# Optimization experiments

Hardware: AMD Instinct MI355X
Metric: run time of the kernel (lower is better)

## Reference

```python
import jax, jax.numpy as jnp
import numpy as np

P, K, T, C, F = 2048, 8, 32, 16384, 128  # paths, channels/path, steps/channel, channels, feature


def setup_inputs() -> dict:
    key = jax.random.key(0)
    k0, k1, k2, k3, k4, k5, k6 = jax.random.split(key, 7)
    s = 1.0 / np.sqrt(F)  # PyTorch GRU init scale
    return {
        "path_h0": jax.random.normal(k0, (P, F), dtype=jnp.float32),
        "channel_features": jax.random.normal(k1, (C, T, F), dtype=jnp.float32) * 0.1,
        "w_ih": jax.random.uniform(k2, (3 * F, F), minval=-s, maxval=s, dtype=jnp.float32),
        "w_hh": jax.random.uniform(k3, (3 * F, F), minval=-s, maxval=s, dtype=jnp.float32),
        "b_ih": jax.random.uniform(k4, (3 * F,), minval=-s, maxval=s, dtype=jnp.float32),
        "b_hh": jax.random.uniform(k5, (3 * F,), minval=-s, maxval=s, dtype=jnp.float32),
        "channel_idx": jax.random.randint(k6, (P, K), 0, C, dtype=jnp.int64),
    }


def reference(path_h0, channel_features, w_ih, w_hh, b_ih, b_hh, channel_idx):
    # Gather each path's K neighbor-channel sequences and concatenate in time:
    # the original code threads the path hidden state through the GRU over each
    # channel sequence in order, which equals one GRU pass over the concatenation.
    seq = channel_features[channel_idx]            # [P, K, T, F]
    p, f = path_h0.shape
    seq = seq.reshape(p, -1, f)                    # [P, K*T, F]
    # Precompute input-gate projections for all timesteps at once.
    x_gates = jnp.einsum("ptf,gf->ptg", seq, w_ih) + b_ih  # [P, K*T, 3F]

    def step(h, xg):
        hg = h @ w_hh.T + b_hh                     # [P, 3F]
        xr, xz, xn = jnp.split(xg, 3, axis=-1)
        hr, hz, hn = jnp.split(hg, 3, axis=-1)
        r = jax.nn.sigmoid(xr + hr)
        z = jax.nn.sigmoid(xz + hz)
        n = jnp.tanh(xn + r * hn)
        h_new = (1.0 - z) * n + z * h              # PyTorch GRU update
        return h_new, None

    h_final, _ = jax.lax.scan(step, path_h0, jnp.swapaxes(x_gates, 0, 1))
    return h_final                                  # [P, F] updated path states
```

## Files before the change

### kernel.cpp

```cpp
#include <hip/hip_runtime.h>
#include <cstdint>
#include <cstddef>

#define PP 2048
#define KK 8
#define TT 32
#define FF 128
#define MB 8
#define NBLK (PP/MB)
#define NTHR 512
#define NSTEP (KK*TT)

typedef __attribute__((ext_vector_type(8))) short short8;
typedef __attribute__((ext_vector_type(4))) float f32x4;

__device__ __forceinline__ uint32_t fbits(float x){ union{float f;uint32_t u;}c;c.f=x;return c.u; }
__device__ __forceinline__ uint32_t rne16(uint32_t u){
    return (u + 0x7fffu + ((u >> 16) & 1u)) >> 16;
}
__device__ __forceinline__ short bf_rne(float x){ return (short)rne16(fbits(x)); }
__device__ __forceinline__ uint32_t pk_rne(float a, float b){
    return rne16(fbits(a)) | (rne16(fbits(b)) << 16);
}
__device__ __forceinline__ float sigm(float x){
    float t = __expf(-x);
    return __builtin_amdgcn_rcpf(1.f + t);
}
__device__ __forceinline__ float tanh_fast(float x){
    float e = __expf(-2.f * x);
    return __builtin_amdgcn_rcpf(1.f + e) * 2.f - 1.f;
}

__global__ __launch_bounds__(NTHR, 2) void gru_mfma5(
    const float* __restrict__ h0,
    const float* __restrict__ feat,
    const float* __restrict__ w_ih,
    const float* __restrict__ w_hh,
    const float* __restrict__ b_ih,
    const float* __restrict__ b_hh,
    const int* __restrict__ idx,
    float* __restrict__ out)
{
    const int tid  = threadIdx.x;
    const int w    = tid >> 6;
    const int lane = tid & 63;
    const int q    = lane >> 4;
    const int nl   = lane & 15;
    const int p0   = blockIdx.x * MB;

    __shared__ __align__(16) short xfr[2][4][32][8];
    __shared__ __align__(16) short hhi[2][4][32][8];
    __shared__ int cix[MB][KK];

    short8 wbi[3][4], wbh[3][4];
#pragma unroll
    for (int tt = 0; tt < 3; ++tt) {
        const int g = (w + 8 * tt) * 16 + nl;
#pragma unroll
        for (int c = 0; c < 4; ++c) {
            const float* wi = w_ih + (size_t)g * FF + c * 32 + q * 8;
            const float* wh = w_hh + (size_t)g * FF + c * 32 + q * 8;
            short8 a, b;
#pragma unroll
            for (int j = 0; j < 8; ++j) { a[j] = bf_rne(wi[j]); b[j] = bf_rne(wh[j]); }
            wbi[tt][c] = a; wbh[tt][c] = b;
        }
    }
    const int fcol = w * 16 + nl;
    const float bR  = b_ih[fcol] + b_hh[fcol];
    const float bZ  = b_ih[FF + fcol] + b_hh[FF + fcol];
    const float bNi = b_ih[2 * FF + fcol];
    const float bNh = b_hh[2 * FF + fcol];

    if (tid < MB * KK) cix[tid >> 3][tid & 7] = idx[(p0 + (tid >> 3)) * KK + (tid & 7)];

    const int qqF = 2 * (w & 1) + (nl >> 3);
    const int jF  = nl & 7;
    const int cF  = w >> 1;
    const int pb  = 4 * (q & 1) + 2 * (q >> 1);
    int sp[2];
#pragma unroll
    for (int j = 0; j < 2; ++j) {
        const int p = pb + j;
        sp[j] = (p >> 2) + 2 * ((p & 3) ^ qqF) + 8 * qqF;
    }

    const int row = lane & 15;
    const int pr  = (row < 8) ? row : ((row & 4) | ((row & 3) ^ 2));
    const int xslot = pr + 8 * q;
    const int hslot = (pr >> 2) + 2 * ((pr & 3) ^ q) + 8 * q;

    float hm[2];
#pragma unroll
    for (int j = 0; j < 2; ++j) {
        const float h = h0[(size_t)(p0 + pb + j) * FF + fcol];
        hm[j] = h;
        hhi[0][cF][sp[j]][jF] = bf_rne(h);
    }

    const bool stg    = tid < 256;
    const int  c_s    = tid >> 6;
    const int  r6     = tid & 63;
    const int  slot_s = r6 >> 1;
    const int  half   = r6 & 1;
    const int  path_s = slot_s & 7;
    const int  qq_s   = slot_s >> 3;
    const int  k0s    = c_s * 32 + qq_s * 8 + 4 * half;

    __syncthreads();

    float4 xp;
    if (stg) {
        const int ch = cix[path_s][0];
        const float* base = feat + (size_t)ch * (TT * FF) + k0s;
        const float4 v0 = *(const float4*)(base);
        const float4 v1 = *(const float4*)(base + FF);
        uint2 p0d = { pk_rne(v0.x, v0.y), pk_rne(v0.z, v0.w) };
        uint2 p1d = { pk_rne(v1.x, v1.y), pk_rne(v1.z, v1.w) };
        *(uint2*)&xfr[0][c_s][slot_s][4 * half] = p0d;
        *(uint2*)&xfr[1][c_s][slot_s][4 * half] = p1d;
        xp = *(const float4*)(base + 2 * FF);
    }
    __syncthreads();

    f32x4 paxR, paxZ, paxN;
    {
        short8 xa0[4];
#pragma unroll
        for (int c = 0; c < 4; ++c) xa0[c] = *(const short8*)&xfr[0][c][xslot][0];
        __syncthreads();

        f32x4 r = {bR, bR, bR, bR}, z = {bZ, bZ, bZ, bZ}, n = {bNi, bNi, bNi, bNi};
#pragma unroll
        for (int c = 0; c < 4; ++c) {
            r = __builtin_amdgcn_mfma_f32_16x16x32_bf16(xa0[c], wbi[0][c], r, 0, 0, 0);
            z = __builtin_amdgcn_mfma_f32_16x16x32_bf16(xa0[c], wbi[1][c], z, 0, 0, 0);
            n = __builtin_amdgcn_mfma_f32_16x16x32_bf16(xa0[c], wbi[2][c], n, 0, 0, 0);
        }
        paxR = r; paxZ = z; paxN = n;
    }

    int curb = 0;
    for (int s = 0; s < NSTEP; ++s) {
        const int nxtb = curb ^ 1;

        if (stg) {
            if (s < NSTEP - 2) {
                uint2 pkd = { pk_rne(xp.x, xp.y), pk_rne(xp.z, xp.w) };
                *(uint2*)&xfr[curb][c_s][slot_s][4 * half] = pkd;
            }
            if (s < NSTEP - 3) {
                const int u = s + 3;
                const int ch = cix[path_s][u >> 5];
                xp = *(const float4*)(feat + (size_t)ch * (TT * FF) + (u & 31) * FF + k0s);
            }
        }

        short8 ha[4];
#pragma unroll
        for (int c = 0; c < 4; ++c) ha[c] = *(const short8*)&hhi[curb][c][hslot][0];
        short8 xn[4];
        if (s < NSTEP - 1) {
#pragma unroll
            for (int c = 0; c < 4; ++c) xn[c] = *(const short8*)&xfr[nxtb][c][xslot][0];
        }

        f32x4 ahN = {bNh, bNh, bNh, bNh};
#pragma unroll
        for (int c = 0; c < 4; ++c) {
            paxR = __builtin_amdgcn_mfma_f32_16x16x32_bf16(ha[c], wbh[0][c], paxR, 0, 0, 0);
            paxZ = __builtin_amdgcn_mfma_f32_16x16x32_bf16(ha[c], wbh[1][c], paxZ, 0, 0, 0);
            ahN  = __builtin_amdgcn_mfma_f32_16x16x32_bf16(ha[c], wbh[2][c], ahN, 0, 0, 0);
        }

#pragma unroll
        for (int j = 0; j < 2; ++j) {
            const float rg  = sigm(paxR[j]);
            const float zg  = sigm(paxZ[j]);
            const float np_ = paxN[j] + rg * ahN[j];
            const float ng  = tanh_fast(np_);
            const float h   = ng + zg * (hm[j] - ng);
            hm[j] = h;
            hhi[nxtb][cF][sp[j]][jF] = bf_rne(h);
        }

        if (s < NSTEP - 1) {
            f32x4 r = {bR, bR, bR, bR}, z = {bZ, bZ, bZ, bZ}, n = {bNi, bNi, bNi, bNi};
#pragma unroll
            for (int c = 0; c < 4; ++c) {
                r = __builtin_amdgcn_mfma_f32_16x16x32_bf16(xn[c], wbi[0][c], r, 0, 0, 0);
                z = __builtin_amdgcn_mfma_f32_16x16x32_bf16(xn[c], wbi[1][c], z, 0, 0, 0);
                n = __builtin_amdgcn_mfma_f32_16x16x32_bf16(xn[c], wbi[2][c], n, 0, 0, 0);
            }
            paxR = r; paxZ = z; paxN = n;
        }

        __syncthreads();
        curb = nxtb;
    }

#pragma unroll
    for (int j = 0; j < 2; ++j)
        out[(size_t)(p0 + pb + j) * FF + fcol] = hm[j];
}

extern "C" void kernel_launch(void* const* d_in, const int* in_sizes, int n_in,
                              void* d_out, int out_size, void* d_ws, size_t ws_size,
                              hipStream_t stream) {
    const float* h0   = (const float*)d_in[0];
    const float* feat = (const float*)d_in[1];
    const float* wih  = (const float*)d_in[2];
    const float* whh  = (const float*)d_in[3];
    const float* bih  = (const float*)d_in[4];
    const float* bhh  = (const float*)d_in[5];
    const int*   idx  = (const int*)d_in[6];
    float*       out  = (float*)d_out;

    gru_mfma5<<<dim3(NBLK), dim3(NTHR), 0, stream>>>(
        h0, feat, wih, whh, bih, bhh, idx, out);
}
```

Before: 480.0 us.

## Batch two timesteps' input projections into one MFMA with 4-deep staging

The recurrence loop now advances two timesteps per iteration. Each MFMA computes the input-gate projections for both steps at once: rows 0-7 hold step s+1 and rows 8-15 hold step s+2. Cross-lane shuffles then route each half to the lane that owns it. This removes the wasted half of the 16-row MFMA tile that only 8 paths filled, so the input projection costs half as many MFMAs per step. The x staging buffer grows to four slots with a deeper prefetch, and bf16 packing switches to the hardware v_cvt_pk_bf16_f32 instruction, which rounds to nearest-even like the old code. The price is extra shuffles and selects plus more register pressure.

```diff
diff --git a/kernel.cpp b/kernel.cpp
--- a/kernel.cpp
+++ b/kernel.cpp
@@ -10,6 +10,7 @@
 #define NBLK (PP/MB)
 #define NTHR 512
 #define NSTEP (KK*TT)
+#define NMAC (NSTEP/2)
 
 typedef __attribute__((ext_vector_type(8))) short short8;
 typedef __attribute__((ext_vector_type(4))) float f32x4;
@@ -19,8 +20,10 @@
     return (u + 0x7fffu + ((u >> 16) & 1u)) >> 16;
 }
 __device__ __forceinline__ short bf_rne(float x){ return (short)rne16(fbits(x)); }
-__device__ __forceinline__ uint32_t pk_rne(float a, float b){
-    return rne16(fbits(a)) | (rne16(fbits(b)) << 16);
+__device__ __forceinline__ uint32_t cvtpk(float a, float b){
+    uint32_t r;
+    asm("v_cvt_pk_bf16_f32 %0, %1, %2" : "=v"(r) : "v"(a), "v"(b));
+    return r;
 }
 __device__ __forceinline__ float sigm(float x){
     float t = __expf(-x);
@@ -31,7 +34,7 @@
     return __builtin_amdgcn_rcpf(1.f + e) * 2.f - 1.f;
 }
 
-__global__ __launch_bounds__(NTHR, 2) void gru_mfma5(
+__global__ __launch_bounds__(NTHR, 2) void gru_mfma6(
     const float* __restrict__ h0,
     const float* __restrict__ feat,
     const float* __restrict__ w_ih,
@@ -48,7 +51,7 @@
     const int nl   = lane & 15;
     const int p0   = blockIdx.x * MB;
 
-    __shared__ __align__(16) short xfr[2][4][32][8];
+    __shared__ __align__(16) short xfr[4][4][32][8];
     __shared__ __align__(16) short hhi[2][4][32][8];
     __shared__ int cix[MB][KK];
 
@@ -78,24 +81,26 @@
     const int jF  = nl & 7;
     const int cF  = w >> 1;
     const int pb  = 4 * (q & 1) + 2 * (q >> 1);
-    int sp[2];
-#pragma unroll
-    for (int j = 0; j < 2; ++j) {
-        const int p = pb + j;
-        sp[j] = (p >> 2) + 2 * ((p & 3) ^ qqF) + 8 * qqF;
+    int sp0, sp1;
+    {
+        const int pA = pb, pB = pb + 1;
+        sp0 = (pA >> 2) + 2 * ((pA & 3) ^ qqF) + 8 * qqF;
+        sp1 = (pB >> 2) + 2 * ((pB & 3) ^ qqF) + 8 * qqF;
     }
 
     const int row = lane & 15;
     const int pr  = (row < 8) ? row : ((row & 4) | ((row & 3) ^ 2));
     const int xslot = pr + 8 * q;
     const int hslot = (pr >> 2) + 2 * ((pr & 3) ^ q) + 8 * q;
-
-    float hm[2];
-#pragma unroll
-    for (int j = 0; j < 2; ++j) {
-        const float h = h0[(size_t)(p0 + pb + j) * FF + fcol];
-        hm[j] = h;
-        hhi[0][cF][sp[j]][jF] = bf_rne(h);
+    const bool rlo = (row < 8);
+    const bool lo  = (lane < 32);
+
+    float hm0 = h0[(size_t)(p0 + pb)     * FF + fcol];
+    float hm1 = h0[(size_t)(p0 + pb + 1) * FF + fcol];
+    {
+        const uint32_t hp = cvtpk(hm0, hm1);
+        hhi[0][cF][sp0][jF] = (short)hp;
+        hhi[0][cF][sp1][jF] = (short)(hp >> 16);
     }
 
     const bool stg    = tid < 256;
@@ -109,27 +114,29 @@
 
     __syncthreads();
 
-    float4 xp;
+    float4 xp0, xp1;
     if (stg) {
         const int ch = cix[path_s][0];
         const float* base = feat + (size_t)ch * (TT * FF) + k0s;
         const float4 v0 = *(const float4*)(base);
         const float4 v1 = *(const float4*)(base + FF);
-        uint2 p0d = { pk_rne(v0.x, v0.y), pk_rne(v0.z, v0.w) };
-        uint2 p1d = { pk_rne(v1.x, v1.y), pk_rne(v1.z, v1.w) };
-        *(uint2*)&xfr[0][c_s][slot_s][4 * half] = p0d;
-        *(uint2*)&xfr[1][c_s][slot_s][4 * half] = p1d;
-        xp = *(const float4*)(base + 2 * FF);
+        const float4 v2 = *(const float4*)(base + 2 * FF);
+        uint2 a0 = { cvtpk(v0.x, v0.y), cvtpk(v0.z, v0.w) };
+        uint2 a1 = { cvtpk(v1.x, v1.y), cvtpk(v1.z, v1.w) };
+        uint2 a2 = { cvtpk(v2.x, v2.y), cvtpk(v2.z, v2.w) };
+        *(uint2*)&xfr[0][c_s][slot_s][4 * half] = a0;
+        *(uint2*)&xfr[1][c_s][slot_s][4 * half] = a1;
+        *(uint2*)&xfr[2][c_s][slot_s][4 * half] = a2;
+        xp0 = *(const float4*)(base + 3 * FF);
+        xp1 = *(const float4*)(base + 4 * FF);
     }
     __syncthreads();
 
-    f32x4 paxR, paxZ, paxN;
+    float xgE[3][2];
     {
         short8 xa0[4];
 #pragma unroll
         for (int c = 0; c < 4; ++c) xa0[c] = *(const short8*)&xfr[0][c][xslot][0];
-        __syncthreads();
-
         f32x4 r = {bR, bR, bR, bR}, z = {bZ, bZ, bZ, bZ}, n = {bNi, bNi, bNi, bNi};
 #pragma unroll
         for (int c = 0; c < 4; ++c) {
@@ -137,71 +144,129 @@
             z = __builtin_amdgcn_mfma_f32_16x16x32_bf16(xa0[c], wbi[1][c], z, 0, 0, 0);
             n = __builtin_amdgcn_mfma_f32_16x16x32_bf16(xa0[c], wbi[2][c], n, 0, 0, 0);
         }
-        paxR = r; paxZ = z; paxN = n;
-    }
-
-    int curb = 0;
-    for (int s = 0; s < NSTEP; ++s) {
-        const int nxtb = curb ^ 1;
+        xgE[0][0] = r[0]; xgE[0][1] = r[1];
+        xgE[1][0] = z[0]; xgE[1][1] = z[1];
+        xgE[2][0] = n[0]; xgE[2][1] = n[1];
+    }
+    __syncthreads();
+
+    for (int m = 0; m < NMAC; ++m) {
+        const int s0 = 2 * m;
+        const int r1  = (s0 + 1) & 3, r2  = (s0 + 2) & 3;
+        const int wr3 = (s0 + 3) & 3, wr4 = (s0 + 4) & 3;
 
         if (stg) {
-            if (s < NSTEP - 2) {
-                uint2 pkd = { pk_rne(xp.x, xp.y), pk_rne(xp.z, xp.w) };
-                *(uint2*)&xfr[curb][c_s][slot_s][4 * half] = pkd;
-            }
-            if (s < NSTEP - 3) {
-                const int u = s + 3;
-                const int ch = cix[path_s][u >> 5];
-                xp = *(const float4*)(feat + (size_t)ch * (TT * FF) + (u & 31) * FF + k0s);
+            if (s0 + 3 < NSTEP) {
+                uint2 pk = { cvtpk(xp0.x, xp0.y), cvtpk(xp0.z, xp0.w) };
+                *(uint2*)&xfr[wr3][c_s][slot_s][4 * half] = pk;
+            }
+            if (s0 + 4 < NSTEP) {
+                uint2 pk = { cvtpk(xp1.x, xp1.y), cvtpk(xp1.z, xp1.w) };
+                *(uint2*)&xfr[wr4][c_s][slot_s][4 * half] = pk;
+            }
+            if (s0 + 5 < NSTEP) {
+                const int u = s0 + 5;
+                xp0 = *(const float4*)(feat + (size_t)cix[path_s][u >> 5] * (TT * FF) + (u & 31) * FF + k0s);
+            }
+            if (s0 + 6 < NSTEP) {
+                const int u = s0 + 6;
+                xp1 = *(const float4*)(feat + (size_t)cix[path_s][u >> 5] * (TT * FF) + (u & 31) * FF + k0s);
             }
         }
 
         short8 ha[4];
 #pragma unroll
-        for (int c = 0; c < 4; ++c) ha[c] = *(const short8*)&hhi[curb][c][hslot][0];
-        short8 xn[4];
-        if (s < NSTEP - 1) {
-#pragma unroll
-            for (int c = 0; c < 4; ++c) xn[c] = *(const short8*)&xfr[nxtb][c][xslot][0];
-        }
-
-        f32x4 ahN = {bNh, bNh, bNh, bNh};
-#pragma unroll
-        for (int c = 0; c < 4; ++c) {
-            paxR = __builtin_amdgcn_mfma_f32_16x16x32_bf16(ha[c], wbh[0][c], paxR, 0, 0, 0);
-            paxZ = __builtin_amdgcn_mfma_f32_16x16x32_bf16(ha[c], wbh[1][c], paxZ, 0, 0, 0);
-            ahN  = __builtin_amdgcn_mfma_f32_16x16x32_bf16(ha[c], wbh[2][c], ahN, 0, 0, 0);
-        }
-
-#pragma unroll
-        for (int j = 0; j < 2; ++j) {
-            const float rg  = sigm(paxR[j]);
-            const float zg  = sigm(paxZ[j]);
-            const float np_ = paxN[j] + rg * ahN[j];
-            const float ng  = tanh_fast(np_);
-            const float h   = ng + zg * (hm[j] - ng);
-            hm[j] = h;
-            hhi[nxtb][cF][sp[j]][jF] = bf_rne(h);
-        }
-
-        if (s < NSTEP - 1) {
-            f32x4 r = {bR, bR, bR, bR}, z = {bZ, bZ, bZ, bZ}, n = {bNi, bNi, bNi, bNi};
+        for (int c = 0; c < 4; ++c) ha[c] = *(const short8*)&hhi[0][c][hslot][0];
+        const short* xbase = rlo ? &xfr[r1][0][0][0] : &xfr[r2][0][0][0];
+        short8 xa[4];
+#pragma unroll
+        for (int c = 0; c < 4; ++c) xa[c] = *(const short8*)(xbase + c * 32 * 8 + xslot * 8);
+
+        {
+            f32x4 aR = {xgE[0][0], xgE[0][1], 0.f, 0.f};
+            f32x4 aZ = {xgE[1][0], xgE[1][1], 0.f, 0.f};
+            f32x4 ahN = {bNh, bNh, bNh, bNh};
 #pragma unroll
             for (int c = 0; c < 4; ++c) {
-                r = __builtin_amdgcn_mfma_f32_16x16x32_bf16(xn[c], wbi[0][c], r, 0, 0, 0);
-                z = __builtin_amdgcn_mfma_f32_16x16x32_bf16(xn[c], wbi[1][c], z, 0, 0, 0);
-                n = __builtin_amdgcn_mfma_f32_16x16x32_bf16(xn[c], wbi[2][c], n, 0, 0, 0);
-            }
-            paxR = r; paxZ = z; paxN = n;
-        }
-
+                aR  = __builtin_amdgcn_mfma_f32_16x16x32_bf16(ha[c], wbh[0][c], aR, 0, 0, 0);
+                aZ  = __builtin_amdgcn_mfma_f32_16x16x32_bf16(ha[c], wbh[1][c], aZ, 0, 0, 0);
+                ahN = __builtin_amdgcn_mfma_f32_16x16x32_bf16(ha[c], wbh[2][c], ahN, 0, 0, 0);
+            }
+#pragma unroll
+            for (int j = 0; j < 2; ++j) {
+                const float rg  = sigm(aR[j]);
+                const float zg  = sigm(aZ[j]);
+                const float np_ = xgE[2][j] + rg * ahN[j];
+                const float ng  = tanh_fast(np_);
+                const float hv  = ng + zg * ((j ? hm1 : hm0) - ng);
+                if (j) hm1 = hv; else hm0 = hv;
+            }
+            const uint32_t hp = cvtpk(hm0, hm1);
+            hhi[1][cF][sp0][jF] = (short)hp;
+            hhi[1][cF][sp1][jF] = (short)(hp >> 16);
+        }
+
+        float xgO[3][2];
+        {
+            f32x4 dR = {bR, bR, bR, bR}, dZ = {bZ, bZ, bZ, bZ}, dN = {bNi, bNi, bNi, bNi};
+#pragma unroll
+            for (int c = 0; c < 4; ++c) {
+                dR = __builtin_amdgcn_mfma_f32_16x16x32_bf16(xa[c], wbi[0][c], dR, 0, 0, 0);
+                dZ = __builtin_amdgcn_mfma_f32_16x16x32_bf16(xa[c], wbi[1][c], dZ, 0, 0, 0);
+                dN = __builtin_amdgcn_mfma_f32_16x16x32_bf16(xa[c], wbi[2][c], dN, 0, 0, 0);
+            }
+            {
+                const float s2 = __shfl_xor(dR[2], 32);
+                const float s3 = __shfl_xor(dR[3], 32);
+                xgO[0][0] = lo ? dR[0] : s2;  xgO[0][1] = lo ? dR[1] : s3;
+                xgE[0][0] = lo ? s2 : dR[0];  xgE[0][1] = lo ? s3 : dR[1];
+            }
+            {
+                const float s2 = __shfl_xor(dZ[2], 32);
+                const float s3 = __shfl_xor(dZ[3], 32);
+                xgO[1][0] = lo ? dZ[0] : s2;  xgO[1][1] = lo ? dZ[1] : s3;
+                xgE[1][0] = lo ? s2 : dZ[0];  xgE[1][1] = lo ? s3 : dZ[1];
+            }
+            {
+                const float s2 = __shfl_xor(dN[2], 32);
+                const float s3 = __shfl_xor(dN[3], 32);
+                xgO[2][0] = lo ? dN[0] : s2;  xgO[2][1] = lo ? dN[1] : s3;
+                xgE[2][0] = lo ? s2 : dN[0];  xgE[2][1] = lo ? s3 : dN[1];
+            }
+        }
         __syncthreads();
-        curb = nxtb;
-    }
-
-#pragma unroll
-    for (int j = 0; j < 2; ++j)
-        out[(size_t)(p0 + pb + j) * FF + fcol] = hm[j];
+
+        {
+            short8 hb[4];
+#pragma unroll
+            for (int c = 0; c < 4; ++c) hb[c] = *(const short8*)&hhi[1][c][hslot][0];
+            f32x4 aR = {xgO[0][0], xgO[0][1], 0.f, 0.f};
+            f32x4 aZ = {xgO[1][0], xgO[1][1], 0.f, 0.f};
+            f32x4 ahN = {bNh, bNh, bNh, bNh};
+#pragma unroll
+            for (int c = 0; c < 4; ++c) {
+                aR  = __builtin_amdgcn_mfma_f32_16x16x32_bf16(hb[c], wbh[0][c], aR, 0, 0, 0);
+                aZ  = __builtin_amdgcn_mfma_f32_16x16x32_bf16(hb[c], wbh[1][c], aZ, 0, 0, 0);
+                ahN = __builtin_amdgcn_mfma_f32_16x16x32_bf16(hb[c], wbh[2][c], ahN, 0, 0, 0);
+            }
+#pragma unroll
+            for (int j = 0; j < 2; ++j) {
+                const float rg  = sigm(aR[j]);
+                const float zg  = sigm(aZ[j]);
+                const float np_ = xgO[2][j] + rg * ahN[j];
+                const float ng  = tanh_fast(np_);
+                const float hv  = ng + zg * ((j ? hm1 : hm0) - ng);
+                if (j) hm1 = hv; else hm0 = hv;
+            }
+            const uint32_t hp = cvtpk(hm0, hm1);
+            hhi[0][cF][sp0][jF] = (short)hp;
+            hhi[0][cF][sp1][jF] = (short)(hp >> 16);
+        }
+        __syncthreads();
+    }
+
+    out[(size_t)(p0 + pb)     * FF + fcol] = hm0;
+    out[(size_t)(p0 + pb + 1) * FF + fcol] = hm1;
 }
 
 extern "C" void kernel_launch(void* const* d_in, const int* in_sizes, int n_in,
@@ -216,6 +281,6 @@
     const int*   idx  = (const int*)d_in[6];
     float*       out  = (float*)d_out;
 
-    gru_mfma5<<<dim3(NBLK), dim3(NTHR), 0, stream>>>(
+    gru_mfma6<<<dim3(NBLK), dim3(NTHR), 0, stream>>>(
         h0, feat, wih, whh, bih, bhh, idx, out);
 }
```

Result: faster. 448.2 us (-6.6%).
